# Optimization experiments

Hardware: AMD Instinct MI355X
Metric: run time of the kernel (lower is better)

Reference implementation:

```python
import jax, jax.numpy as jnp
import numpy as np

EPS = 1e-08


def setup_inputs() -> dict:
    key = jax.random.key(0)
    k_x, k_w1, k_b1, k_w2, k_b2 = jax.random.split(key, 5)
    B, C, T = 64, 64, 4000
    x = jax.random.normal(k_x, (B, C, T, 1), dtype=jnp.float32)
    # 1x1 Conv2D with in_channels=1, out_channels=8 -> weight is an 8-vector + bias
    w1 = jax.random.normal(k_w1, (8,), dtype=jnp.float32) * 0.5
    b1 = jax.random.normal(k_b1, (8,), dtype=jnp.float32) * 0.1
    w2 = jax.random.normal(k_w2, (8,), dtype=jnp.float32) * 0.5
    b2 = jax.random.normal(k_b2, (8,), dtype=jnp.float32) * 0.1
    # gamma is initialized to 0 in the module (residual identity at init);
    # use a nonzero value so the attention path is exercised numerically.
    gamma = jnp.float32(0.5)
    return {"x": x, "w1": w1, "b1": b1, "w2": w2, "b2": b2, "gamma": gamma}


def reference(x, w1, b1, w2, b2, gamma):
    B, C, T, _ = x.shape  # (B, num_ch, T, 1)
    # 1x1 conv with C_in=1: broadcast multiply-add, then flatten (T, 8) -> T*8
    q = (x * w1 + b1).reshape(B, C, T * 8)  # proj_query (B, C, T*8)
    k = (x * w2 + b2).reshape(B, C, T * 8)  # proj_key   (B, C, T*8)
    # energy = Q @ K^T  -> (B, C, C)
    energy = jnp.einsum('bcd,bed->bce', q, k)
    # custom min-max normalization along last axis, then softmax
    max_h = jnp.max(energy, axis=2, keepdims=True)
    min_h = jnp.min(energy, axis=2, keepdims=True)
    energy = (energy - min_h) / (max_h - min_h + EPS)
    attention = jax.nn.softmax(energy, axis=-1)
    xs = x[..., 0]  # squeeze last dim -> (B, C, T)
    # attention^T @ xs  (transpose_a=True)
    attended = jnp.einsum('bec,bet->bct', attention, xs)
    return gamma * attended[..., None] + x
```

## Files before the change

### kernel.cpp

```cpp
#include <hip/hip_runtime.h>

#define BB 64
#define CC 64
#define TT 4000

#define SLABS 8
#define TSLAB 250
#define SLABT (2 * TSLAB)
#define GP_PITCH 264

#define TPB 128
#define XPITCH 132
#define APITCH 72

#define GPART_ELEMS ((size_t)SLABS * BB * CC * CC)

typedef short short8 __attribute__((ext_vector_type(8)));
typedef float f32x16 __attribute__((ext_vector_type(16)));

__device__ __forceinline__ short f2bf(float f) {
    unsigned u = __float_as_uint(f);
    u = (u + 0x7FFFu + ((u >> 16) & 1u)) >> 16;
    return (short)u;
}
__device__ __forceinline__ float bfpair(unsigned u) {
    return __uint_as_float(u << 16) + __uint_as_float(u & 0xFFFF0000u);
}

__global__ __launch_bounds__(256)
void gram_mfma(const float* __restrict__ x, float* __restrict__ G_part,
               float* __restrict__ S_part) {
    __shared__ short xs[CC * GP_PITCH];
    __shared__ float sred[4 * 64];
    const int b    = blockIdx.x / SLABS;
    const int slab = blockIdx.x % SLABS;
    const int tid  = threadIdx.x;
    const int lane = tid & 63;
    const int wave = tid >> 6;
    const float* xb = x + (size_t)b * CC * TT;

    const int r0 = (wave >> 1) * 32, c0 = (wave & 1) * 32;
    const int m = lane & 31, half = lane >> 5;
    f32x16 acc;
    #pragma unroll
    for (int z = 0; z < 16; ++z) acc[z] = 0.f;
    float s_acc = 0.f;

    for (int ch = 0; ch < 2; ++ch) {
        const int t0 = slab * SLABT + ch * TSLAB;

        #pragma unroll
        for (int g = 0; g < 2; ++g) {
            float4 v[8];
            #pragma unroll
            for (int k = 0; k < 8; ++k) {
                const int i = tid + 256 * (g * 8 + k);
                const int row = i >> 6, tq = i & 63;
                float4 w = make_float4(0.f, 0.f, 0.f, 0.f);
                if (tq < 62) {
                    w = *(const float4*)(xb + row * TT + t0 + 4 * tq);
                } else if (tq == 62) {
                    const float* p = xb + row * TT + t0 + 248;
                    w.x = p[0]; w.y = p[1];
                }
                v[k] = w;
            }
            #pragma unroll
            for (int k = 0; k < 8; ++k) {
                const int i = tid + 256 * (g * 8 + k);
                const int row = i >> 6, tq = i & 63;
                short4 sv;
                sv.x = f2bf(v[k].x); sv.y = f2bf(v[k].y);
                sv.z = f2bf(v[k].z); sv.w = f2bf(v[k].w);
                const int pc = (tq >> 1) ^ (row & 7);
                *(short4*)(xs + row * GP_PITCH + pc * 8 + (tq & 1) * 4) = sv;
            }
        }
        __syncthreads();

        {
            const short* rowp = xs + lane * GP_PITCH;
            #pragma unroll
            for (int j = 0; j < 8; ++j) {
                const int pc = (wave * 8 + j) ^ (lane & 7);
                uint2 u0 = *(const uint2*)(rowp + pc * 8);
                uint2 u1 = *(const uint2*)(rowp + pc * 8 + 4);
                s_acc += bfpair(u0.x) + bfpair(u0.y) + bfpair(u1.x) + bfpair(u1.y);
            }
        }

        #pragma unroll
        for (int ks = 0; ks < 16; ++ks) {
            const int ck = ks * 2 + half;
            short8 av = *(const short8*)(xs + (r0 + m) * GP_PITCH + (ck ^ (m & 7)) * 8);
            short8 bv = *(const short8*)(xs + (c0 + m) * GP_PITCH + (ck ^ (m & 7)) * 8);
            acc = __builtin_amdgcn_mfma_f32_32x32x16_bf16(av, bv, acc, 0, 0, 0);
        }
        __syncthreads();
    }

    sred[wave * 64 + lane] = s_acc;
    __syncthreads();
    if (tid < 64) {
        float s = sred[tid] + sred[64 + tid] + sred[128 + tid] + sred[192 + tid];
        S_part[(slab * BB + b) * CC + tid] = s;
    }

    float* gp = G_part + ((size_t)slab * BB + b) * (CC * CC);
    #pragma unroll
    for (int r = 0; r < 16; ++r) {
        const int row = (r & 3) + 8 * (r >> 2) + 4 * half;
        gp[(r0 + row) * CC + (c0 + m)] = acc[r];
    }
}

__global__ __launch_bounds__(256)
void softmax_apply(const float* __restrict__ x,
                   const float* __restrict__ w1, const float* __restrict__ b1,
                   const float* __restrict__ w2, const float* __restrict__ b2,
                   const float* __restrict__ G_part, const float* __restrict__ S_part,
                   const float* __restrict__ gamma, float* __restrict__ out) {
    __shared__ float xsbuf[CC * XPITCH];
    __shared__ short al[CC * APITCH];
    __shared__ float red[3 * 256];
    __shared__ float Sb[64];
    const int tid  = threadIdx.x;
    const int lane = tid & 63, wave = tid >> 6;
    const int b    = blockIdx.x & 63;
    const int slab = blockIdx.x >> 6;
    const float* xb = x + (size_t)b * CC * TT;
    const int m = lane & 31, half = lane >> 5;

    {
        float* Es = xsbuf;
        #pragma unroll
        for (int j4 = 0; j4 < 4; ++j4) {
            const int jj = tid + 256 * j4;
            float4 s = make_float4(0.f, 0.f, 0.f, 0.f);
            #pragma unroll
            for (int sl = 0; sl < SLABS; ++sl) {
                const float4 g = *(const float4*)(G_part + ((size_t)sl * BB + b) * 4096 + 4 * jj);
                s.x += g.x; s.y += g.y; s.z += g.z; s.w += g.w;
            }
            const int row = jj >> 4, col = (jj & 15) * 4;
            float* e = Es + row * 65 + col;
            e[0] = s.x; e[1] = s.y; e[2] = s.z; e[3] = s.w;
        }
        if (tid < 64) {
            float s = 0.f;
            #pragma unroll
            for (int sl = 0; sl < SLABS; ++sl)
                s += S_part[(sl * BB + b) * CC + tid];
            Sb[tid] = s;
        }
        float A = 0.f, Bc = 0.f, Be = 0.f, Cc = 0.f;
        #pragma unroll
        for (int j = 0; j < 8; ++j) {
            float a1 = w1[j], a2 = w2[j], q1 = b1[j], q2 = b2[j];
            A += a1 * a2; Bc += a1 * q2; Be += q1 * a2; Cc += q1 * q2;
        }
        Cc *= (float)TT;
        __syncthreads();

        const int c = tid & 63, q = tid >> 6;
        const float sc = Sb[c];
        float ev[16], mn = 1e30f, mx = -1e30f;
        #pragma unroll
        for (int i = 0; i < 16; ++i) {
            const int e = 16 * q + i;
            float en = A * Es[c * 65 + e] + Bc * sc + Be * Sb[e] + Cc;
            ev[i] = en;
            mn = fminf(mn, en); mx = fmaxf(mx, en);
        }
        red[q * 64 + c] = mn; red[256 + q * 64 + c] = mx;
        __syncthreads();
        mn = fminf(fminf(red[c], red[64 + c]), fminf(red[128 + c], red[192 + c]));
        mx = fmaxf(fmaxf(red[256 + c], red[320 + c]), fmaxf(red[384 + c], red[448 + c]));
        const float ninv = 1.f / (mx - mn + 1e-8f);
        float pv[16], ls = 0.f;
        #pragma unroll
        for (int i = 0; i < 16; ++i) {
            float p = __expf((ev[i] - mn) * ninv);
            pv[i] = p; ls += p;
        }
        red[512 + q * 64 + c] = ls;
        __syncthreads();
        const float rinv = 1.f / (red[512 + c] + red[576 + c] + red[640 + c] + red[704 + c]);
        #pragma unroll
        for (int i = 0; i < 16; ++i)
            al[(16 * q + i) * APITCH + c] = f2bf(pv[i] * rinv);
        __syncthreads();
    }

    {
        const int c0 = (wave & 1) * 32;
        const int tb = (wave >> 1) * 64;
        const float gm = gamma[0];
        float* ob = out + (size_t)b * CC * TT;
        const int t0s = slab * SLABT;

        for (int it = 0; it < 4; ++it) {
            const int t0l = it * TPB;
            const int t0  = t0s + t0l;
            #pragma unroll
            for (int g2 = 0; g2 < 2; ++g2) {
                float4 v[4];
                #pragma unroll
                for (int k = 0; k < 4; ++k) {
                    const int i = tid + 256 * (g2 * 4 + k);
                    const int e = i >> 5, p = i & 31;
                    const int t = t0 + 4 * p;
                    v[k] = make_float4(0.f, 0.f, 0.f, 0.f);
                    if (t < TT) v[k] = *(const float4*)(xb + e * TT + t);
                }
                #pragma unroll
                for (int k = 0; k < 4; ++k) {
                    const int i = tid + 256 * (g2 * 4 + k);
                    const int e = i >> 5, p = i & 31;
                    *(float4*)(xsbuf + e * XPITCH + 4 * p) = v[k];
                }
            }
            __syncthreads();

            f32x16 acc0, acc1;
            #pragma unroll
            for (int z = 0; z < 16; ++z) { acc0[z] = 0.f; acc1[z] = 0.f; }
            #pragma unroll
            for (int ks = 0; ks < 4; ++ks) {
                short8 av = *(const short8*)(al + (c0 + m) * APITCH + ks * 16 + 8 * half);
                const int eb = ks * 16 + 8 * half;
                short8 bv0, bv1;
                #pragma unroll
                for (int j = 0; j < 8; ++j) {
                    bv0[j] = f2bf(xsbuf[(eb + j) * XPITCH + tb + m]);
                    bv1[j] = f2bf(xsbuf[(eb + j) * XPITCH + tb + 32 + m]);
                }
                acc0 = __builtin_amdgcn_mfma_f32_32x32x16_bf16(av, bv0, acc0, 0, 0, 0);
                acc1 = __builtin_amdgcn_mfma_f32_32x32x16_bf16(av, bv1, acc1, 0, 0, 0);
            }

            #pragma unroll
            for (int r = 0; r < 16; ++r) {
                const int row = (r & 3) + 8 * (r >> 2) + 4 * half;
                const int c = c0 + row;
                const int tl0 = tb + m, tl1 = tb + 32 + m;
                if (t0l + tl0 < SLABT)
                    ob[c * TT + t0 + tl0] = gm * acc0[r] + xsbuf[c * XPITCH + tl0];
                if (t0l + tl1 < SLABT)
                    ob[c * TT + t0 + tl1] = gm * acc1[r] + xsbuf[c * XPITCH + tl1];
            }
            __syncthreads();
        }
    }
}

extern "C" void kernel_launch(void* const* d_in, const int* in_sizes, int n_in,
                              void* d_out, int out_size, void* d_ws, size_t ws_size,
                              hipStream_t stream) {
    const float* x  = (const float*)d_in[0];
    const float* w1 = (const float*)d_in[1];
    const float* b1 = (const float*)d_in[2];
    const float* w2 = (const float*)d_in[3];
    const float* b2 = (const float*)d_in[4];
    const float* gm = (const float*)d_in[5];
    float* out = (float*)d_out;

    float* G_part = (float*)d_ws;
    float* S_part = G_part + GPART_ELEMS;

    hipLaunchKernelGGL(gram_mfma, dim3(BB * SLABS), dim3(256), 0, stream,
                       x, G_part, S_part);
    hipLaunchKernelGGL(softmax_apply, dim3(BB * SLABS), dim3(256), 0, stream,
                       x, w1, b1, w2, b2, G_part, S_part, gm, out);
}
```

Baseline: 157.4 us.

## Double-buffer gram staging and read x directly from global in apply

The gram kernel now uses two LDS buffers and issues the global loads for the second time chunk before running the MFMA and row-sum work on the first, so load latency overlaps with compute. The apply kernel drops its LDS staging of x and the barriers around it, reading x straight from global memory (scalar, coalesced across lanes) for both the MFMA B operand and the residual add. The attention A fragments are also hoisted out of the time loop into registers. In exchange, gram LDS use doubles and more registers are live, which may cut occupancy, and apply now issues many scalar global loads, re-reading each x element for the residual and relying on cache hits.

```diff
diff --git a/kernel.cpp b/kernel.cpp
--- a/kernel.cpp
+++ b/kernel.cpp
@@ -10,7 +10,6 @@
 #define GP_PITCH 264
 
 #define TPB 128
-#define XPITCH 132
 #define APITCH 72
 
 #define GPART_ELEMS ((size_t)SLABS * BB * CC * CC)
@@ -27,10 +26,61 @@
     return __uint_as_float(u << 16) + __uint_as_float(u & 0xFFFF0000u);
 }
 
+__device__ __forceinline__ void stage_load(const float* __restrict__ xb, int t0,
+                                           int g, int tid, float4 v[8]) {
+    #pragma unroll
+    for (int k = 0; k < 8; ++k) {
+        const int i = tid + 256 * (g * 8 + k);
+        const int row = i >> 6, tq = i & 63;
+        float4 w = make_float4(0.f, 0.f, 0.f, 0.f);
+        if (tq < 62) {
+            w = *(const float4*)(xb + row * TT + t0 + 4 * tq);
+        } else if (tq == 62) {
+            const float* p = xb + row * TT + t0 + 248;
+            w.x = p[0]; w.y = p[1];
+        }
+        v[k] = w;
+    }
+}
+__device__ __forceinline__ void stage_write(short* xs, int g, int tid, const float4 v[8]) {
+    #pragma unroll
+    for (int k = 0; k < 8; ++k) {
+        const int i = tid + 256 * (g * 8 + k);
+        const int row = i >> 6, tq = i & 63;
+        short4 sv;
+        sv.x = f2bf(v[k].x); sv.y = f2bf(v[k].y);
+        sv.z = f2bf(v[k].z); sv.w = f2bf(v[k].w);
+        const int pc = (tq >> 1) ^ (row & 7);
+        *(short4*)(xs + row * GP_PITCH + pc * 8 + (tq & 1) * 4) = sv;
+    }
+}
+__device__ __forceinline__ float s_partial(const short* xs, int lane, int wave) {
+    const short* rowp = xs + lane * GP_PITCH;
+    float s = 0.f;
+    #pragma unroll
+    for (int j = 0; j < 8; ++j) {
+        const int pc = (wave * 8 + j) ^ (lane & 7);
+        uint2 u0 = *(const uint2*)(rowp + pc * 8);
+        uint2 u1 = *(const uint2*)(rowp + pc * 8 + 4);
+        s += bfpair(u0.x) + bfpair(u0.y) + bfpair(u1.x) + bfpair(u1.y);
+    }
+    return s;
+}
+__device__ __forceinline__ void mfma_tile(const short* xs, int r0, int c0,
+                                          int m, int half, f32x16& acc) {
+    #pragma unroll
+    for (int ks = 0; ks < 16; ++ks) {
+        const int ck = ks * 2 + half;
+        short8 av = *(const short8*)(xs + (r0 + m) * GP_PITCH + (ck ^ (m & 7)) * 8);
+        short8 bv = *(const short8*)(xs + (c0 + m) * GP_PITCH + (ck ^ (m & 7)) * 8);
+        acc = __builtin_amdgcn_mfma_f32_32x32x16_bf16(av, bv, acc, 0, 0, 0);
+    }
+}
+
 __global__ __launch_bounds__(256)
 void gram_mfma(const float* __restrict__ x, float* __restrict__ G_part,
                float* __restrict__ S_part) {
-    __shared__ short xs[CC * GP_PITCH];
+    __shared__ short xs[2][CC * GP_PITCH];
     __shared__ float sred[4 * 64];
     const int b    = blockIdx.x / SLABS;
     const int slab = blockIdx.x % SLABS;
@@ -44,60 +94,31 @@
     f32x16 acc;
     #pragma unroll
     for (int z = 0; z < 16; ++z) acc[z] = 0.f;
-    float s_acc = 0.f;
-
-    for (int ch = 0; ch < 2; ++ch) {
-        const int t0 = slab * SLABT + ch * TSLAB;
-
-        #pragma unroll
-        for (int g = 0; g < 2; ++g) {
-            float4 v[8];
-            #pragma unroll
-            for (int k = 0; k < 8; ++k) {
-                const int i = tid + 256 * (g * 8 + k);
-                const int row = i >> 6, tq = i & 63;
-                float4 w = make_float4(0.f, 0.f, 0.f, 0.f);
-                if (tq < 62) {
-                    w = *(const float4*)(xb + row * TT + t0 + 4 * tq);
-                } else if (tq == 62) {
-                    const float* p = xb + row * TT + t0 + 248;
-                    w.x = p[0]; w.y = p[1];
-                }
-                v[k] = w;
-            }
-            #pragma unroll
-            for (int k = 0; k < 8; ++k) {
-                const int i = tid + 256 * (g * 8 + k);
-                const int row = i >> 6, tq = i & 63;
-                short4 sv;
-                sv.x = f2bf(v[k].x); sv.y = f2bf(v[k].y);
-                sv.z = f2bf(v[k].z); sv.w = f2bf(v[k].w);
-                const int pc = (tq >> 1) ^ (row & 7);
-                *(short4*)(xs + row * GP_PITCH + pc * 8 + (tq & 1) * 4) = sv;
-            }
-        }
-        __syncthreads();
-
-        {
-            const short* rowp = xs + lane * GP_PITCH;
-            #pragma unroll
-            for (int j = 0; j < 8; ++j) {
-                const int pc = (wave * 8 + j) ^ (lane & 7);
-                uint2 u0 = *(const uint2*)(rowp + pc * 8);
-                uint2 u1 = *(const uint2*)(rowp + pc * 8 + 4);
-                s_acc += bfpair(u0.x) + bfpair(u0.y) + bfpair(u1.x) + bfpair(u1.y);
-            }
-        }
-
-        #pragma unroll
-        for (int ks = 0; ks < 16; ++ks) {
-            const int ck = ks * 2 + half;
-            short8 av = *(const short8*)(xs + (r0 + m) * GP_PITCH + (ck ^ (m & 7)) * 8);
-            short8 bv = *(const short8*)(xs + (c0 + m) * GP_PITCH + (ck ^ (m & 7)) * 8);
-            acc = __builtin_amdgcn_mfma_f32_32x32x16_bf16(av, bv, acc, 0, 0, 0);
-        }
-        __syncthreads();
-    }
+
+    const int t0a = slab * SLABT, t0b = t0a + TSLAB;
+
+    {
+        float4 v[8];
+        stage_load(xb, t0a, 0, tid, v);
+        stage_write(xs[0], 0, tid, v);
+        stage_load(xb, t0a, 1, tid, v);
+        stage_write(xs[0], 1, tid, v);
+    }
+    __syncthreads();
+
+    float4 p0[8], p1[8];
+    stage_load(xb, t0b, 0, tid, p0);
+    stage_load(xb, t0b, 1, tid, p1);
+
+    float s_acc = s_partial(xs[0], lane, wave);
+    mfma_tile(xs[0], r0, c0, m, half, acc);
+
+    stage_write(xs[1], 0, tid, p0);
+    stage_write(xs[1], 1, tid, p1);
+    __syncthreads();
+
+    s_acc += s_partial(xs[1], lane, wave);
+    mfma_tile(xs[1], r0, c0, m, half, acc);
 
     sred[wave * 64 + lane] = s_acc;
     __syncthreads();
@@ -105,7 +126,6 @@
         float s = sred[tid] + sred[64 + tid] + sred[128 + tid] + sred[192 + tid];
         S_part[(slab * BB + b) * CC + tid] = s;
     }
-
     float* gp = G_part + ((size_t)slab * BB + b) * (CC * CC);
     #pragma unroll
     for (int r = 0; r < 16; ++r) {
@@ -120,7 +140,7 @@
                    const float* __restrict__ w2, const float* __restrict__ b2,
                    const float* __restrict__ G_part, const float* __restrict__ S_part,
                    const float* __restrict__ gamma, float* __restrict__ out) {
-    __shared__ float xsbuf[CC * XPITCH];
+    __shared__ float Es[64 * 65];
     __shared__ short al[CC * APITCH];
     __shared__ float red[3 * 256];
     __shared__ float Sb[64];
@@ -132,7 +152,6 @@
     const int m = lane & 31, half = lane >> 5;
 
     {
-        float* Es = xsbuf;
         #pragma unroll
         for (int j4 = 0; j4 < 4; ++j4) {
             const int jj = tid + 256 * j4;
@@ -195,61 +214,48 @@
     {
         const int c0 = (wave & 1) * 32;
         const int tb = (wave >> 1) * 64;
+        short8 av[4];
+        #pragma unroll
+        for (int ks = 0; ks < 4; ++ks)
+            av[ks] = *(const short8*)(al + (c0 + m) * APITCH + ks * 16 + 8 * half);
+
         const float gm = gamma[0];
         float* ob = out + (size_t)b * CC * TT;
         const int t0s = slab * SLABT;
 
         for (int it = 0; it < 4; ++it) {
-            const int t0l = it * TPB;
-            const int t0  = t0s + t0l;
-            #pragma unroll
-            for (int g2 = 0; g2 < 2; ++g2) {
-                float4 v[4];
-                #pragma unroll
-                for (int k = 0; k < 4; ++k) {
-                    const int i = tid + 256 * (g2 * 4 + k);
-                    const int e = i >> 5, p = i & 31;
-                    const int t = t0 + 4 * p;
-                    v[k] = make_float4(0.f, 0.f, 0.f, 0.f);
-                    if (t < TT) v[k] = *(const float4*)(xb + e * TT + t);
-                }
-                #pragma unroll
-                for (int k = 0; k < 4; ++k) {
-                    const int i = tid + 256 * (g2 * 4 + k);
-                    const int e = i >> 5, p = i & 31;
-                    *(float4*)(xsbuf + e * XPITCH + 4 * p) = v[k];
-                }
-            }
-            __syncthreads();
-
+            const int t0 = t0s + it * TPB;
+            const int ta = t0 + tb + m;
+            const int tc = ta + 32;
             f32x16 acc0, acc1;
             #pragma unroll
             for (int z = 0; z < 16; ++z) { acc0[z] = 0.f; acc1[z] = 0.f; }
+
             #pragma unroll
             for (int ks = 0; ks < 4; ++ks) {
-                short8 av = *(const short8*)(al + (c0 + m) * APITCH + ks * 16 + 8 * half);
                 const int eb = ks * 16 + 8 * half;
                 short8 bv0, bv1;
                 #pragma unroll
                 for (int j = 0; j < 8; ++j) {
-                    bv0[j] = f2bf(xsbuf[(eb + j) * XPITCH + tb + m]);
-                    bv1[j] = f2bf(xsbuf[(eb + j) * XPITCH + tb + 32 + m]);
+                    const float xa = (ta < TT) ? xb[(eb + j) * TT + ta] : 0.f;
+                    const float xc = (tc < TT) ? xb[(eb + j) * TT + tc] : 0.f;
+                    bv0[j] = f2bf(xa);
+                    bv1[j] = f2bf(xc);
                 }
-                acc0 = __builtin_amdgcn_mfma_f32_32x32x16_bf16(av, bv0, acc0, 0, 0, 0);
-                acc1 = __builtin_amdgcn_mfma_f32_32x32x16_bf16(av, bv1, acc1, 0, 0, 0);
+                acc0 = __builtin_amdgcn_mfma_f32_32x32x16_bf16(av[ks], bv0, acc0, 0, 0, 0);
+                acc1 = __builtin_amdgcn_mfma_f32_32x32x16_bf16(av[ks], bv1, acc1, 0, 0, 0);
             }
 
+            const int tl0 = it * TPB + tb + m;
             #pragma unroll
             for (int r = 0; r < 16; ++r) {
                 const int row = (r & 3) + 8 * (r >> 2) + 4 * half;
                 const int c = c0 + row;
-                const int tl0 = tb + m, tl1 = tb + 32 + m;
-                if (t0l + tl0 < SLABT)
-                    ob[c * TT + t0 + tl0] = gm * acc0[r] + xsbuf[c * XPITCH + tl0];
-                if (t0l + tl1 < SLABT)
-                    ob[c * TT + t0 + tl1] = gm * acc1[r] + xsbuf[c * XPITCH + tl1];
+                if (tl0 < SLABT)
+                    ob[c * TT + ta] = gm * acc0[r] + xb[c * TT + ta];
+                if (tl0 + 32 < SLABT)
+                    ob[c * TT + tc] = gm * acc1[r] + xb[c * TT + tc];
             }
-            __syncthreads();
         }
     }
 }
```

New measurement: 184.3 us. 1.17x slower.

## Fuse gram and apply kernels via grid barrier, reuse bf16 x slab in LDS

Applied to the files above, without the earlier changes.

Merges the Gram-matrix kernel and the softmax/apply kernel into one kernel whose 512 workgroups synchronise through a global atomic spin barrier. Each workgroup keeps its full 500-column x slab in LDS as bf16, so the apply phase no longer re-reads x from global memory. The residual term is also taken from this bf16 copy. The change also adds packed bf16 conversion and hoists the attention MFMA operands out of the time loop. In exchange it relies on all workgroups being co-resident for the barrier, adds a memset launch, and loses precision in the residual add.

```diff
diff --git a/kernel.cpp b/kernel.cpp
--- a/kernel.cpp
+++ b/kernel.cpp
@@ -5,15 +5,13 @@
 #define TT 4000
 
 #define SLABS 8
-#define TSLAB 250
-#define SLABT (2 * TSLAB)
-#define GP_PITCH 264
-
-#define TPB 128
-#define XPITCH 132
+#define SLABT 500
+#define NWG   (BB * SLABS)
+#define XS_PITCH 520
 #define APITCH 72
 
 #define GPART_ELEMS ((size_t)SLABS * BB * CC * CC)
+#define SPART_ELEMS ((size_t)SLABS * BB * CC)
 
 typedef short short8 __attribute__((ext_vector_type(8)));
 typedef float f32x16 __attribute__((ext_vector_type(16)));
@@ -23,129 +21,112 @@
     u = (u + 0x7FFFu + ((u >> 16) & 1u)) >> 16;
     return (short)u;
 }
+__device__ __forceinline__ unsigned cvt_pk(float a, float b) {
+    unsigned r;
+    asm("v_cvt_pk_bf16_f32 %0, %1, %2" : "=v"(r) : "v"(a), "v"(b));
+    return r;
+}
 __device__ __forceinline__ float bfpair(unsigned u) {
     return __uint_as_float(u << 16) + __uint_as_float(u & 0xFFFF0000u);
 }
-
-__global__ __launch_bounds__(256)
-void gram_mfma(const float* __restrict__ x, float* __restrict__ G_part,
-               float* __restrict__ S_part) {
-    __shared__ short xs[CC * GP_PITCH];
-    __shared__ float sred[4 * 64];
-    const int b    = blockIdx.x / SLABS;
-    const int slab = blockIdx.x % SLABS;
-    const int tid  = threadIdx.x;
-    const int lane = tid & 63;
-    const int wave = tid >> 6;
-    const float* xb = x + (size_t)b * CC * TT;
-
-    const int r0 = (wave >> 1) * 32, c0 = (wave & 1) * 32;
-    const int m = lane & 31, half = lane >> 5;
-    f32x16 acc;
-    #pragma unroll
-    for (int z = 0; z < 16; ++z) acc[z] = 0.f;
-    float s_acc = 0.f;
-
-    for (int ch = 0; ch < 2; ++ch) {
-        const int t0 = slab * SLABT + ch * TSLAB;
-
-        #pragma unroll
-        for (int g = 0; g < 2; ++g) {
-            float4 v[8];
-            #pragma unroll
-            for (int k = 0; k < 8; ++k) {
-                const int i = tid + 256 * (g * 8 + k);
-                const int row = i >> 6, tq = i & 63;
-                float4 w = make_float4(0.f, 0.f, 0.f, 0.f);
-                if (tq < 62) {
-                    w = *(const float4*)(xb + row * TT + t0 + 4 * tq);
-                } else if (tq == 62) {
-                    const float* p = xb + row * TT + t0 + 248;
-                    w.x = p[0]; w.y = p[1];
-                }
-                v[k] = w;
-            }
-            #pragma unroll
-            for (int k = 0; k < 8; ++k) {
-                const int i = tid + 256 * (g * 8 + k);
-                const int row = i >> 6, tq = i & 63;
-                short4 sv;
-                sv.x = f2bf(v[k].x); sv.y = f2bf(v[k].y);
-                sv.z = f2bf(v[k].z); sv.w = f2bf(v[k].w);
-                const int pc = (tq >> 1) ^ (row & 7);
-                *(short4*)(xs + row * GP_PITCH + pc * 8 + (tq & 1) * 4) = sv;
-            }
-        }
-        __syncthreads();
-
-        {
-            const short* rowp = xs + lane * GP_PITCH;
-            #pragma unroll
-            for (int j = 0; j < 8; ++j) {
-                const int pc = (wave * 8 + j) ^ (lane & 7);
-                uint2 u0 = *(const uint2*)(rowp + pc * 8);
-                uint2 u1 = *(const uint2*)(rowp + pc * 8 + 4);
-                s_acc += bfpair(u0.x) + bfpair(u0.y) + bfpair(u1.x) + bfpair(u1.y);
-            }
-        }
-
-        #pragma unroll
-        for (int ks = 0; ks < 16; ++ks) {
-            const int ck = ks * 2 + half;
-            short8 av = *(const short8*)(xs + (r0 + m) * GP_PITCH + (ck ^ (m & 7)) * 8);
-            short8 bv = *(const short8*)(xs + (c0 + m) * GP_PITCH + (ck ^ (m & 7)) * 8);
-            acc = __builtin_amdgcn_mfma_f32_32x32x16_bf16(av, bv, acc, 0, 0, 0);
-        }
-        __syncthreads();
-    }
-
-    sred[wave * 64 + lane] = s_acc;
-    __syncthreads();
-    if (tid < 64) {
-        float s = sred[tid] + sred[64 + tid] + sred[128 + tid] + sred[192 + tid];
-        S_part[(slab * BB + b) * CC + tid] = s;
-    }
-
-    float* gp = G_part + ((size_t)slab * BB + b) * (CC * CC);
-    #pragma unroll
-    for (int r = 0; r < 16; ++r) {
-        const int row = (r & 3) + 8 * (r >> 2) + 4 * half;
-        gp[(r0 + row) * CC + (c0 + m)] = acc[r];
-    }
-}
-
-__global__ __launch_bounds__(256)
-void softmax_apply(const float* __restrict__ x,
-                   const float* __restrict__ w1, const float* __restrict__ b1,
-                   const float* __restrict__ w2, const float* __restrict__ b2,
-                   const float* __restrict__ G_part, const float* __restrict__ S_part,
-                   const float* __restrict__ gamma, float* __restrict__ out) {
-    __shared__ float xsbuf[CC * XPITCH];
+__device__ __forceinline__ float bf2f(short s) {
+    return __uint_as_float(((unsigned)(unsigned short)s) << 16);
+}
+
+__global__ __launch_bounds__(256, 2)
+void fused_attn(const float* __restrict__ x,
+                const float* __restrict__ w1, const float* __restrict__ b1,
+                const float* __restrict__ w2, const float* __restrict__ b2,
+                const float* __restrict__ gamma,
+                float* __restrict__ G_part, float* __restrict__ S_part,
+                unsigned* __restrict__ bar, float* __restrict__ out) {
+    __shared__ short xs[CC * XS_PITCH];
     __shared__ short al[CC * APITCH];
     __shared__ float red[3 * 256];
     __shared__ float Sb[64];
+
     const int tid  = threadIdx.x;
     const int lane = tid & 63, wave = tid >> 6;
     const int b    = blockIdx.x & 63;
     const int slab = blockIdx.x >> 6;
+    const int t0s  = slab * SLABT;
     const float* xb = x + (size_t)b * CC * TT;
     const int m = lane & 31, half = lane >> 5;
+    const int r0 = (wave >> 1) * 32, c0w = (wave & 1) * 32;
+
+    #pragma unroll
+    for (int g = 0; g < 4; ++g) {
+        float4 v[8];
+        #pragma unroll
+        for (int k = 0; k < 8; ++k) {
+            const int i = tid + 256 * (g * 8 + k);
+            const int row = i >> 7, tq = i & 127;
+            float4 w = make_float4(0.f, 0.f, 0.f, 0.f);
+            if (tq < 125) w = *(const float4*)(xb + row * TT + t0s + 4 * tq);
+            v[k] = w;
+        }
+        #pragma unroll
+        for (int k = 0; k < 8; ++k) {
+            const int i = tid + 256 * (g * 8 + k);
+            const int row = i >> 7, tq = i & 127;
+            uint2 sv;
+            sv.x = cvt_pk(v[k].x, v[k].y);
+            sv.y = cvt_pk(v[k].z, v[k].w);
+            const int pc = (tq >> 1) ^ (row & 7);
+            *(uint2*)(xs + row * XS_PITCH + pc * 8 + (tq & 1) * 4) = sv;
+        }
+    }
+    __syncthreads();
 
     {
-        float* Es = xsbuf;
-        #pragma unroll
-        for (int j4 = 0; j4 < 4; ++j4) {
-            const int jj = tid + 256 * j4;
-            float4 s = make_float4(0.f, 0.f, 0.f, 0.f);
-            #pragma unroll
-            for (int sl = 0; sl < SLABS; ++sl) {
-                const float4 g = *(const float4*)(G_part + ((size_t)sl * BB + b) * 4096 + 4 * jj);
-                s.x += g.x; s.y += g.y; s.z += g.z; s.w += g.w;
-            }
-            const int row = jj >> 4, col = (jj & 15) * 4;
-            float* e = Es + row * 65 + col;
-            e[0] = s.x; e[1] = s.y; e[2] = s.z; e[3] = s.w;
-        }
+        float s_acc = 0.f;
+        const short* rowp = xs + lane * XS_PITCH;
+        #pragma unroll
+        for (int j = 0; j < 16; ++j) {
+            const int pc = (wave * 16 + j) ^ (lane & 7);
+            uint2 u0 = *(const uint2*)(rowp + pc * 8);
+            uint2 u1 = *(const uint2*)(rowp + pc * 8 + 4);
+            s_acc += bfpair(u0.x) + bfpair(u0.y) + bfpair(u1.x) + bfpair(u1.y);
+        }
+        f32x16 acc;
+        #pragma unroll
+        for (int z = 0; z < 16; ++z) acc[z] = 0.f;
+        #pragma unroll
+        for (int ks = 0; ks < 32; ++ks) {
+            const int ck = ks * 2 + half;
+            short8 av = *(const short8*)(xs + (r0 + m) * XS_PITCH + (ck ^ (m & 7)) * 8);
+            short8 bv = *(const short8*)(xs + (c0w + m) * XS_PITCH + (ck ^ (m & 7)) * 8);
+            acc = __builtin_amdgcn_mfma_f32_32x32x16_bf16(av, bv, acc, 0, 0, 0);
+        }
+        red[wave * 64 + lane] = s_acc;
+        __syncthreads();
+        if (tid < 64) {
+            float s = red[tid] + red[64 + tid] + red[128 + tid] + red[192 + tid];
+            S_part[(slab * BB + b) * CC + tid] = s;
+        }
+        float* gp = G_part + ((size_t)slab * BB + b) * (CC * CC);
+        #pragma unroll
+        for (int r = 0; r < 16; ++r) {
+            const int row = (r & 3) + 8 * (r >> 2) + 4 * half;
+            gp[(r0 + row) * CC + (c0w + m)] = acc[r];
+        }
+    }
+
+    __threadfence();
+    __syncthreads();
+    if (tid == 0) {
+        __hip_atomic_fetch_add(bar, 1u, __ATOMIC_ACQ_REL, __HIP_MEMORY_SCOPE_AGENT);
+        unsigned it = 0;
+        while (__hip_atomic_load(bar, __ATOMIC_ACQUIRE, __HIP_MEMORY_SCOPE_AGENT) < NWG) {
+            __builtin_amdgcn_s_sleep(2);
+            if (++it > (1u << 26)) break;
+        }
+    }
+    __syncthreads();
+    __threadfence();
+
+    {
+        const int c = lane, q = wave;
         if (tid < 64) {
             float s = 0.f;
             #pragma unroll
@@ -160,15 +141,30 @@
             A += a1 * a2; Bc += a1 * q2; Be += q1 * a2; Cc += q1 * q2;
         }
         Cc *= (float)TT;
-        __syncthreads();
-
-        const int c = tid & 63, q = tid >> 6;
+
+        float g16[16];
+        #pragma unroll
+        for (int i = 0; i < 16; ++i) g16[i] = 0.f;
+        const float* gb = G_part + (size_t)b * (CC * CC) + c * 64 + 16 * q;
+        #pragma unroll
+        for (int sl = 0; sl < SLABS; ++sl) {
+            const float* p = gb + (size_t)sl * BB * (CC * CC);
+            float4 v0 = *(const float4*)(p);
+            float4 v1 = *(const float4*)(p + 4);
+            float4 v2 = *(const float4*)(p + 8);
+            float4 v3 = *(const float4*)(p + 12);
+            g16[0]  += v0.x; g16[1]  += v0.y; g16[2]  += v0.z; g16[3]  += v0.w;
+            g16[4]  += v1.x; g16[5]  += v1.y; g16[6]  += v1.z; g16[7]  += v1.w;
+            g16[8]  += v2.x; g16[9]  += v2.y; g16[10] += v2.z; g16[11] += v2.w;
+            g16[12] += v3.x; g16[13] += v3.y; g16[14] += v3.z; g16[15] += v3.w;
+        }
+        __syncthreads();
+
         const float sc = Sb[c];
         float ev[16], mn = 1e30f, mx = -1e30f;
         #pragma unroll
         for (int i = 0; i < 16; ++i) {
-            const int e = 16 * q + i;
-            float en = A * Es[c * 65 + e] + Bc * sc + Be * Sb[e] + Cc;
+            float en = A * g16[i] + Bc * sc + Be * Sb[16 * q + i] + Cc;
             ev[i] = en;
             mn = fminf(mn, en); mx = fmaxf(mx, en);
         }
@@ -193,63 +189,52 @@
     }
 
     {
-        const int c0 = (wave & 1) * 32;
-        const int tb = (wave >> 1) * 64;
+        short8 av[4];
+        #pragma unroll
+        for (int ks = 0; ks < 4; ++ks)
+            av[ks] = *(const short8*)(al + (c0w + m) * APITCH + ks * 16 + 8 * half);
+
         const float gm = gamma[0];
         float* ob = out + (size_t)b * CC * TT;
-        const int t0s = slab * SLABT;
-
+        const int tb = (wave >> 1) * 64;
+
+        #pragma unroll
         for (int it = 0; it < 4; ++it) {
-            const int t0l = it * TPB;
-            const int t0  = t0s + t0l;
-            #pragma unroll
-            for (int g2 = 0; g2 < 2; ++g2) {
-                float4 v[4];
-                #pragma unroll
-                for (int k = 0; k < 4; ++k) {
-                    const int i = tid + 256 * (g2 * 4 + k);
-                    const int e = i >> 5, p = i & 31;
-                    const int t = t0 + 4 * p;
-                    v[k] = make_float4(0.f, 0.f, 0.f, 0.f);
-                    if (t < TT) v[k] = *(const float4*)(xb + e * TT + t);
-                }
-                #pragma unroll
-                for (int k = 0; k < 4; ++k) {
-                    const int i = tid + 256 * (g2 * 4 + k);
-                    const int e = i >> 5, p = i & 31;
-                    *(float4*)(xsbuf + e * XPITCH + 4 * p) = v[k];
-                }
-            }
-            __syncthreads();
-
+            const int tl0 = it * 128 + tb + m;
+            const int tl1 = tl0 + 32;
+            const int cq0 = tl0 >> 3, cq1 = tl1 >> 3, el = tl0 & 7;
             f32x16 acc0, acc1;
             #pragma unroll
             for (int z = 0; z < 16; ++z) { acc0[z] = 0.f; acc1[z] = 0.f; }
+
             #pragma unroll
             for (int ks = 0; ks < 4; ++ks) {
-                short8 av = *(const short8*)(al + (c0 + m) * APITCH + ks * 16 + 8 * half);
-                const int eb = ks * 16 + 8 * half;
                 short8 bv0, bv1;
                 #pragma unroll
                 for (int j = 0; j < 8; ++j) {
-                    bv0[j] = f2bf(xsbuf[(eb + j) * XPITCH + tb + m]);
-                    bv1[j] = f2bf(xsbuf[(eb + j) * XPITCH + tb + 32 + m]);
+                    const int e = ks * 16 + 8 * half + j;
+                    const short* rp = xs + e * XS_PITCH;
+                    bv0[j] = rp[((cq0 ^ (e & 7)) << 3) + el];
+                    bv1[j] = rp[((cq1 ^ (e & 7)) << 3) + el];
                 }
-                acc0 = __builtin_amdgcn_mfma_f32_32x32x16_bf16(av, bv0, acc0, 0, 0, 0);
-                acc1 = __builtin_amdgcn_mfma_f32_32x32x16_bf16(av, bv1, acc1, 0, 0, 0);
+                acc0 = __builtin_amdgcn_mfma_f32_32x32x16_bf16(av[ks], bv0, acc0, 0, 0, 0);
+                acc1 = __builtin_amdgcn_mfma_f32_32x32x16_bf16(av[ks], bv1, acc1, 0, 0, 0);
             }
 
             #pragma unroll
             for (int r = 0; r < 16; ++r) {
                 const int row = (r & 3) + 8 * (r >> 2) + 4 * half;
-                const int c = c0 + row;
-                const int tl0 = tb + m, tl1 = tb + 32 + m;
-                if (t0l + tl0 < SLABT)
-                    ob[c * TT + t0 + tl0] = gm * acc0[r] + xsbuf[c * XPITCH + tl0];
-                if (t0l + tl1 < SLABT)
-                    ob[c * TT + t0 + tl1] = gm * acc1[r] + xsbuf[c * XPITCH + tl1];
+                const int cc2 = c0w + row;
+                const short* rp = xs + cc2 * XS_PITCH;
+                if (tl0 < SLABT) {
+                    const float res = bf2f(rp[((cq0 ^ (cc2 & 7)) << 3) + el]);
+                    ob[cc2 * TT + t0s + tl0] = gm * acc0[r] + res;
+                }
+                if (tl1 < SLABT) {
+                    const float res = bf2f(rp[((cq1 ^ (cc2 & 7)) << 3) + el]);
+                    ob[cc2 * TT + t0s + tl1] = gm * acc1[r] + res;
+                }
             }
-            __syncthreads();
         }
     }
 }
@@ -267,9 +252,9 @@
 
     float* G_part = (float*)d_ws;
     float* S_part = G_part + GPART_ELEMS;
-
-    hipLaunchKernelGGL(gram_mfma, dim3(BB * SLABS), dim3(256), 0, stream,
-                       x, G_part, S_part);
-    hipLaunchKernelGGL(softmax_apply, dim3(BB * SLABS), dim3(256), 0, stream,
-                       x, w1, b1, w2, b2, G_part, S_part, gm, out);
-}
+    unsigned* bar = (unsigned*)(S_part + SPART_ELEMS);
+
+    hipMemsetAsync(bar, 0, sizeof(unsigned), stream);
+    hipLaunchKernelGGL(fused_attn, dim3(NWG), dim3(256), 0, stream,
+                       x, w1, b1, w2, b2, gm, G_part, S_part, bar, out);
+}
```

Result: slower. 242.7 us (+54.3%).
